# Kernel tuning notes

Measured on AMD Instinct MI355X. Metric: run time of the kernel, lower is better.

## Reference

```python
import jax, jax.numpy as jnp
import numpy as np

N, E, H = 50000, 800000, 128

def _lin_params(key, out_dim, in_dim, bias=True, gain=1.0):
    k1, k2 = jax.random.split(key)
    lim = gain * np.sqrt(6.0 / (in_dim + out_dim))
    W = jax.random.uniform(k1, (out_dim, in_dim), jnp.float32, -lim, lim)
    b = jax.random.uniform(k2, (out_dim,), jnp.float32, -lim, lim) if bias else None
    return W, b

def setup_inputs() -> dict:
    key = jax.random.key(0)
    ks = jax.random.split(key, 12)
    h = jax.random.normal(ks[0], (N, H), jnp.float32)
    x = jax.random.normal(ks[1], (N, 3), jnp.float32)
    edge_index = jax.random.randint(ks[2], (2, E), 0, N, jnp.int64)
    We1, be1 = _lin_params(ks[3], H, 2 * H + 1)
    We2, be2 = _lin_params(ks[4], H, H)
    Wn1, bn1 = _lin_params(ks[5], H, 2 * H)
    Wn2, bn2 = _lin_params(ks[6], H, H)
    Wc1, bc1 = _lin_params(ks[7], H, H)
    Wc2, _ = _lin_params(ks[8], 1, H, bias=False, gain=0.001)
    gamma = jnp.ones((H,), jnp.float32)
    beta = jnp.zeros((H,), jnp.float32)
    return {"h": h, "x": x, "edge_index": edge_index,
            "We1": We1, "be1": be1, "We2": We2, "be2": be2,
            "Wn1": Wn1, "bn1": bn1, "Wn2": Wn2, "bn2": bn2,
            "Wc1": Wc1, "bc1": bc1, "Wc2": Wc2,
            "gamma": gamma, "beta": beta}

def _layer_norm(y, gamma, beta, eps=1e-5):
    mu = jnp.mean(y, axis=-1, keepdims=True)
    var = jnp.var(y, axis=-1, keepdims=True)
    return (y - mu) * jax.lax.rsqrt(var + eps) * gamma + beta

def reference(h, x, edge_index, We1, be1, We2, be2, Wn1, bn1, Wn2, bn2,
              Wc1, bc1, Wc2, gamma, beta):
    src, dst = edge_index[0], edge_index[1]
    diff = x[src] - x[dst]                                  # (E, 3)
    dist_sq = jnp.sum(diff * diff, axis=-1, keepdims=True)  # (E, 1)
    edge_in = jnp.concatenate([h[src], h[dst], dist_sq], axis=-1)  # (E, 2H+1)
    m = jax.nn.silu(edge_in @ We1.T + be1)
    m = jax.nn.silu(m @ We2.T + be2)                        # (E, H)
    num_nodes = h.shape[0]
    agg = jax.ops.segment_sum(m, dst, num_segments=num_nodes)            # (N, H)
    count = jax.ops.segment_sum(jnp.ones((dst.shape[0], 1), h.dtype), dst,
                                num_segments=num_nodes)
    count = jnp.maximum(count, 1.0)
    agg = agg / count
    u = jax.nn.silu(jnp.concatenate([h, agg], axis=-1) @ Wn1.T + bn1)
    h_out = h + (u @ Wn2.T + bn2)
    h_out = _layer_norm(h_out, gamma, beta)
    cw = jax.nn.silu(m @ Wc1.T + bc1) @ Wc2.T               # (E, 1)
    coord_agg = jax.ops.segment_sum(diff * cw, dst, num_segments=num_nodes) / count
    x_out = x + coord_agg
    return h_out, x_out
```

## Files before the change

### kernel.cpp

```cpp
#include <hip/hip_runtime.h>
#include <stdint.h>

using bf16x8 = __attribute__((ext_vector_type(8))) short;
using f32x4  = __attribute__((ext_vector_type(4))) float;

__device__ __forceinline__ unsigned short f2bf(float f) {
  uint32_t x = __float_as_uint(f);
  x += 0x7fffu + ((x >> 16) & 1u);
  return (unsigned short)(x >> 16);
}
__device__ __forceinline__ float bf2f(unsigned short u) {
  return __uint_as_float(((uint32_t)u) << 16);
}
__device__ __forceinline__ uint32_t cvtpk2(float lo, float hi) {
  uint32_t r;
  asm("v_cvt_pk_bf16_f32 %0, %1, %2" : "=v"(r) : "v"(lo), "v"(hi));
  return r;
}
__device__ __forceinline__ float silu_f(float v) {
  float e = __expf(-v);
  return v * __builtin_amdgcn_rcpf(1.0f + e);
}
__device__ __forceinline__ void unpack2(uint32_t u, float& lo, float& hi) {
  lo = __uint_as_float(u << 16);
  hi = __uint_as_float(u & 0xffff0000u);
}

__device__ __forceinline__ int msoff(int row, int col) {
  return row * 136 + ((((col >> 3) + row * 4) & 15) << 3) + (col & 7);
}
__device__ __forceinline__ int msoff_slot(int row, int slot) {
  return row * 136 + (((slot + row * 4) & 15) << 3);
}

__global__ void prep_kernel(const float* __restrict__ We1, const float* __restrict__ We2,
                            const float* __restrict__ Wn1, const float* __restrict__ Wn2,
                            const float* __restrict__ Wc1, const int* __restrict__ ei,
                            unsigned short* __restrict__ W1p, unsigned short* __restrict__ W2b,
                            unsigned short* __restrict__ N1b, unsigned short* __restrict__ N2b,
                            unsigned short* __restrict__ W3b, float* __restrict__ w1c,
                            int* __restrict__ flag) {
  int i = blockIdx.x * 256 + threadIdx.x;
  if (i < 256 * 128) {
    int c = i >> 7, k = i & 127;
    W1p[i] = f2bf(We1[(size_t)(c & 127) * 257 + ((c >> 7) << 7) + k]);
    N1b[i] = f2bf(Wn1[i]);
  }
  if (i < 128 * 128) {
    W2b[i] = f2bf(We2[i]);
    W3b[i] = f2bf(Wc1[i]);
    N2b[i] = f2bf(Wn2[i]);
  }
  if (i < 128) w1c[i] = We1[i * 257 + 256];
  if (i == 0) {
    int allz = 1;
    for (int k = 0; k < 64; ++k) allz &= (ei[2 * k + 1] == 0);
    *flag = allz;
  }
}

__global__ void hist_kernel(const int* __restrict__ ei, const int* __restrict__ flag,
                            int* __restrict__ deg, int E) {
  int e0 = (blockIdx.x * 256 + threadIdx.x) * 2;
  if (e0 >= E) return;
  bool has1 = (e0 + 1 < E);
  int d0, d1 = 0;
  if (*flag) {
    const long long* p = (const long long*)ei + E + e0;
    d0 = (int)p[0]; if (has1) d1 = (int)p[1];
  } else {
    const int* p = ei + E + e0;
    d0 = p[0]; if (has1) d1 = p[1];
  }
  atomicAdd(&deg[d0], 1);
  if (has1) atomicAdd(&deg[d1], 1);
}

__global__ void scanA_kernel(const int* __restrict__ deg, int* __restrict__ offs,
                             int* __restrict__ bsum, int N) {
  __shared__ int sh[256];
  int t = threadIdx.x, idx = blockIdx.x * 256 + t;
  int v = (idx < N) ? deg[idx] : 0;
  sh[t] = v;
  __syncthreads();
#pragma unroll
  for (int d = 1; d < 256; d <<= 1) {
    int u = (t >= d) ? sh[t - d] : 0;
    __syncthreads();
    sh[t] += u;
    __syncthreads();
  }
  if (idx < N) offs[idx] = sh[t] - v;
  if (t == 255) bsum[blockIdx.x] = sh[255];
}

__global__ void scanB_kernel(int* __restrict__ bsum, int* __restrict__ offs,
                             int nb, int N) {
  __shared__ int sh[256];
  int t = threadIdx.x;
  int v = (t < nb) ? bsum[t] : 0;
  sh[t] = v;
  __syncthreads();
#pragma unroll
  for (int d = 1; d < 256; d <<= 1) {
    int u = (t >= d) ? sh[t - d] : 0;
    __syncthreads();
    sh[t] += u;
    __syncthreads();
  }
  bsum[t] = sh[t] - v;
  if (t == 255) offs[N] = sh[255];
}

__global__ void scanC_kernel(const int* __restrict__ bsum, int* __restrict__ offs,
                             int* __restrict__ cursor, int N) {
  int idx = blockIdx.x * 256 + threadIdx.x;
  if (idx < N) {
    int o = offs[idx] + bsum[blockIdx.x];
    offs[idx] = o;
    cursor[idx] = o;
  }
}

__global__ void scatter_kernel(const int* __restrict__ ei, const int* __restrict__ flag,
                               int* __restrict__ cursor, int2* __restrict__ sd_s, int E) {
  int e0 = (blockIdx.x * 256 + threadIdx.x) * 2;
  if (e0 >= E) return;
  int ne = min(2, E - e0);
  int ss[2], dd[2];
  if (*flag) {
    const long long* ps = (const long long*)ei + e0;
    const long long* pd = (const long long*)ei + E + e0;
    for (int j = 0; j < ne; ++j) { ss[j] = (int)ps[j]; dd[j] = (int)pd[j]; }
  } else {
    const int* ps = ei + e0;
    const int* pd = ei + E + e0;
    for (int j = 0; j < ne; ++j) { ss[j] = ps[j]; dd[j] = pd[j]; }
  }
  for (int j = 0; j < ne; ++j) {
    int pos = atomicAdd(&cursor[dd[j]], 1);
    int2 p; p.x = ss[j]; p.y = dd[j];
    sd_s[pos] = p;
  }
}

__global__ __launch_bounds__(256) void proj_kernel(
    const float* __restrict__ h, const float* __restrict__ be1,
    const unsigned short* __restrict__ W1p,
    unsigned short* __restrict__ Ps, unsigned short* __restrict__ Pd, int N) {
  const int tid = threadIdx.x;
  const int base = blockIdx.x * 64;
  const int w = tid >> 6, lane = tid & 63, lg = lane >> 4, lr = lane & 15;

  f32x4 acc[4][4];
#pragma unroll
  for (int m = 0; m < 4; ++m)
#pragma unroll
    for (int n = 0; n < 4; ++n) { f32x4 z = {0.f,0.f,0.f,0.f}; acc[m][n] = z; }

#pragma unroll
  for (int k0 = 0; k0 < 4; ++k0) {
    bf16x8 b[4];
#pragma unroll
    for (int n = 0; n < 4; ++n)
      b[n] = *(const bf16x8*)(W1p + ((w * 64 + n * 16 + lr) << 7) + k0 * 32 + lg * 8);
#pragma unroll
    for (int m = 0; m < 4; ++m) {
      int row = base + m * 16 + lr; if (row >= N) row = N - 1;
      const float* p = h + (size_t)row * 128 + k0 * 32 + lg * 8;
      float4 fa = *(const float4*)p;
      float4 fb = *(const float4*)(p + 4);
      union { uint32_t u[4]; bf16x8 v; } cv;
      cv.u[0] = cvtpk2(fa.x, fa.y); cv.u[1] = cvtpk2(fa.z, fa.w);
      cv.u[2] = cvtpk2(fb.x, fb.y); cv.u[3] = cvtpk2(fb.z, fb.w);
#pragma unroll
      for (int n = 0; n < 4; ++n)
        acc[m][n] = __builtin_amdgcn_mfma_f32_16x16x32_bf16(cv.v, b[n], acc[m][n], 0, 0, 0);
    }
  }
#pragma unroll
  for (int n = 0; n < 4; ++n) {
    int o = w * 64 + n * 16 + lr;
    unsigned short* dstp = (o < 128) ? Ps : Pd;
    int oo = o & 127;
    float add = (o < 128) ? be1[o] : 0.f;
#pragma unroll
    for (int m = 0; m < 4; ++m)
#pragma unroll
      for (int r = 0; r < 4; ++r) {
        int row = base + m * 16 + lg * 4 + r;
        if (row < N) dstp[(size_t)row * 128 + oo] = f2bf(acc[m][n][r] + add);
      }
  }
}

__global__ __launch_bounds__(256, 6) void edge_kernel(
    const unsigned short* __restrict__ Ps, const unsigned short* __restrict__ Pd,
    const float* __restrict__ x, const int2* __restrict__ sd_s,
    const int* __restrict__ offs,
    const float* __restrict__ w1c,
    const float* __restrict__ be2, const float* __restrict__ bc1,
    const float* __restrict__ Wc2,
    const unsigned short* __restrict__ W2b, const unsigned short* __restrict__ W3b,
    float* __restrict__ aggH, float* __restrict__ coordX, int E) {
  __shared__ __align__(16) unsigned short Ms[64 * 136];
  __shared__ float swred[4][64];
  __shared__ int   ssrc[64], sdst[64];
  __shared__ float sds[64];
  __shared__ float sdif[64][3];
  __shared__ unsigned char sA[64], sB[64];

  const int tid   = threadIdx.x;
  const int tbase = blockIdx.x * 64;
  const int w = tid >> 6, lane = tid & 63, lg = lane >> 4, lr = lane & 15;

  if (tid < 64) {
    int p0 = tbase + tid;
    int s = 0, d = 0;
    unsigned char fa = 0, fb = 0;
    if (p0 < E) {
      int2 p = sd_s[p0]; s = p.x; d = p.y;
      fa = (offs[d] == p0);
      fb = (offs[d + 1] == p0 + 1);
    }
    ssrc[tid] = s; sdst[tid] = d;
    sA[tid] = fa; sB[tid] = fb;
    float dx = x[s * 3 + 0] - x[d * 3 + 0];
    float dy = x[s * 3 + 1] - x[d * 3 + 1];
    float dz = x[s * 3 + 2] - x[d * 3 + 2];
    sdif[tid][0] = dx; sdif[tid][1] = dy; sdif[tid][2] = dz;
    sds[tid] = dx * dx + dy * dy + dz * dz;
  }
  __syncthreads();

  {
    const float4* w4 = (const float4*)w1c;
#pragma unroll
    for (int ch = 0; ch < 2; ++ch) {
      uint4 av[2], bv[2];
#pragma unroll
      for (int it = 0; it < 2; ++it) {
        int idx = tid + (ch * 2 + it) * 256;
        int e = idx >> 4, seg = idx & 15;
        av[it] = *(const uint4*)(Ps + (size_t)ssrc[e] * 128 + seg * 8);
        bv[it] = *(const uint4*)(Pd + (size_t)sdst[e] * 128 + seg * 8);
      }
#pragma unroll
      for (int it = 0; it < 2; ++it) {
        int idx = tid + (ch * 2 + it) * 256;
        int e = idx >> 4, seg = idx & 15;
        float dsv = sds[e];
        float4 wA = w4[seg * 2], wB = w4[seg * 2 + 1];
        float a0,a1,a2,a3,a4,a5,a6,a7, b0,b1,b2,b3,b4,b5,b6,b7;
        unpack2(((uint32_t*)&av[it])[0], a0, a1);
        unpack2(((uint32_t*)&av[it])[1], a2, a3);
        unpack2(((uint32_t*)&av[it])[2], a4, a5);
        unpack2(((uint32_t*)&av[it])[3], a6, a7);
        unpack2(((uint32_t*)&bv[it])[0], b0, b1);
        unpack2(((uint32_t*)&bv[it])[1], b2, b3);
        unpack2(((uint32_t*)&bv[it])[2], b4, b5);
        unpack2(((uint32_t*)&bv[it])[3], b6, b7);
        float v0 = silu_f(a0 + b0 + dsv * wA.x);
        float v1 = silu_f(a1 + b1 + dsv * wA.y);
        float v2 = silu_f(a2 + b2 + dsv * wA.z);
        float v3 = silu_f(a3 + b3 + dsv * wA.w);
        float v4 = silu_f(a4 + b4 + dsv * wB.x);
        float v5 = silu_f(a5 + b5 + dsv * wB.y);
        float v6 = silu_f(a6 + b6 + dsv * wB.z);
        float v7 = silu_f(a7 + b7 + dsv * wB.w);
        uint4 o;
        o.x = cvtpk2(v0, v1); o.y = cvtpk2(v2, v3);
        o.z = cvtpk2(v4, v5); o.w = cvtpk2(v6, v7);
        *(uint4*)(&Ms[msoff_slot(e, seg)]) = o;
      }
    }
  }
  __syncthreads();

  {
    f32x4 acc[4][2];
#pragma unroll
    for (int m = 0; m < 4; ++m) { f32x4 z = {0.f,0.f,0.f,0.f}; acc[m][0] = z; acc[m][1] = z; }
#pragma unroll
    for (int k0 = 0; k0 < 4; ++k0) {
      bf16x8 b0 = *(const bf16x8*)(W2b + ((w * 32 + lr)      << 7) + k0 * 32 + lg * 8);
      bf16x8 b1 = *(const bf16x8*)(W2b + ((w * 32 + 16 + lr) << 7) + k0 * 32 + lg * 8);
#pragma unroll
      for (int m = 0; m < 4; ++m) {
        int row = m * 16 + lr;
        bf16x8 a = *(const bf16x8*)(&Ms[msoff_slot(row, k0 * 4 + lg)]);
        acc[m][0] = __builtin_amdgcn_mfma_f32_16x16x32_bf16(a, b0, acc[m][0], 0, 0, 0);
        acc[m][1] = __builtin_amdgcn_mfma_f32_16x16x32_bf16(a, b1, acc[m][1], 0, 0, 0);
      }
    }
    uint32_t pk[4][2][2];
#pragma unroll
    for (int n = 0; n < 2; ++n) {
      int o = w * 32 + n * 16 + lr;
      float b2v = be2[o];
#pragma unroll
      for (int m = 0; m < 4; ++m)
#pragma unroll
        for (int r2 = 0; r2 < 4; r2 += 2)
          pk[m][n][r2 >> 1] = cvtpk2(silu_f(acc[m][n][r2] + b2v),
                                     silu_f(acc[m][n][r2 + 1] + b2v));
    }
    __syncthreads();
#pragma unroll
    for (int n = 0; n < 2; ++n) {
      int o = w * 32 + n * 16 + lr;
#pragma unroll
      for (int m = 0; m < 4; ++m)
#pragma unroll
        for (int r2 = 0; r2 < 4; r2 += 2) {
          int row = m * 16 + lg * 4 + r2;
          uint32_t u = pk[m][n][r2 >> 1];
          Ms[msoff(row, o)]     = (unsigned short)(u & 0xffffu);
          Ms[msoff(row + 1, o)] = (unsigned short)(u >> 16);
        }
    }
  }
  __syncthreads();

  {
    f32x4 acc[4][2];
#pragma unroll
    for (int m = 0; m < 4; ++m) { f32x4 z = {0.f,0.f,0.f,0.f}; acc[m][0] = z; acc[m][1] = z; }
#pragma unroll
    for (int k0 = 0; k0 < 4; ++k0) {
      bf16x8 b0 = *(const bf16x8*)(W3b + ((w * 32 + lr)      << 7) + k0 * 32 + lg * 8);
      bf16x8 b1 = *(const bf16x8*)(W3b + ((w * 32 + 16 + lr) << 7) + k0 * 32 + lg * 8);
#pragma unroll
      for (int m = 0; m < 4; ++m) {
        int row = m * 16 + lr;
        bf16x8 a = *(const bf16x8*)(&Ms[msoff_slot(row, k0 * 4 + lg)]);
        acc[m][0] = __builtin_amdgcn_mfma_f32_16x16x32_bf16(a, b0, acc[m][0], 0, 0, 0);
        acc[m][1] = __builtin_amdgcn_mfma_f32_16x16x32_bf16(a, b1, acc[m][1], 0, 0, 0);
      }
    }
    float pr[4][4];
#pragma unroll
    for (int m = 0; m < 4; ++m)
#pragma unroll
      for (int r2 = 0; r2 < 4; ++r2) pr[m][r2] = 0.f;
#pragma unroll
    for (int n = 0; n < 2; ++n) {
      int o = w * 32 + n * 16 + lr;
      float b3 = bc1[o], wc = Wc2[o];
#pragma unroll
      for (int m = 0; m < 4; ++m)
#pragma unroll
        for (int r2 = 0; r2 < 4; ++r2)
          pr[m][r2] += silu_f(acc[m][n][r2] + b3) * wc;
    }
#pragma unroll
    for (int m = 0; m < 4; ++m)
#pragma unroll
      for (int r2 = 0; r2 < 4; ++r2) {
        float v = pr[m][r2];
        v += __shfl_xor(v, 1); v += __shfl_xor(v, 2);
        v += __shfl_xor(v, 4); v += __shfl_xor(v, 8);
        pr[m][r2] = v;
      }
    if (lr == 0) {
#pragma unroll
      for (int m = 0; m < 4; ++m)
#pragma unroll
        for (int r2 = 0; r2 < 4; ++r2)
          swred[w][m * 16 + lg * 4 + r2] = pr[m][r2];
    }
  }
  __syncthreads();

  const int nv = min(64, E - tbase);
  if (tid < 128) {
    int cp = tid & 63, hf = tid >> 6;
    int c0 = cp * 2;
    int e0 = hf * 32;
    int nvh = min(32, nv - e0);
    if (nvh > 0) {
      float r0 = 0.f, r1 = 0.f;
      int prev = sdst[e0];
      int es = e0;
#pragma unroll 4
      for (int j = 0; j < nvh; ++j) {
        int e = e0 + j;
        int d = sdst[e];
        uint32_t u = *(const uint32_t*)(&Ms[msoff(e, c0)]);
        if (d != prev) {
          float* a0 = &aggH[(size_t)prev * 128 + c0];
          if (sA[es] && sB[e - 1]) { a0[0] = r0; a0[1] = r1; }
          else { atomicAdd(a0, r0); atomicAdd(a0 + 1, r1); }
          r0 = 0.f; r1 = 0.f; prev = d; es = e;
        }
        float lo, hi; unpack2(u, lo, hi);
        r0 += lo; r1 += hi;
      }
      float* a0 = &aggH[(size_t)prev * 128 + c0];
      if (sA[es] && sB[e0 + nvh - 1]) { a0[0] = r0; a0[1] = r1; }
      else { atomicAdd(a0, r0); atomicAdd(a0 + 1, r1); }
    }
  } else if (tid >= 192 && tid < 198) {
    int t6 = tid - 192;
    int c3 = t6 % 3, hf = t6 / 3;
    int e0 = hf * 32;
    int nvh = min(32, nv - e0);
    if (nvh > 0) {
      float run = 0.f;
      int prev = sdst[e0];
      int es = e0;
#pragma unroll 4
      for (int j = 0; j < nvh; ++j) {
        int e = e0 + j;
        int d = sdst[e];
        float cwv = swred[0][e] + swred[1][e] + swred[2][e] + swred[3][e];
        if (d != prev) {
          if (sA[es] && sB[e - 1]) coordX[(size_t)prev * 3 + c3] = run;
          else atomicAdd(&coordX[(size_t)prev * 3 + c3], run);
          run = 0.f; prev = d; es = e;
        }
        run += sdif[e][c3] * cwv;
      }
      if (sA[es] && sB[e0 + nvh - 1]) coordX[(size_t)prev * 3 + c3] = run;
      else atomicAdd(&coordX[(size_t)prev * 3 + c3], run);
    }
  }
}

__global__ __launch_bounds__(256) void node_kernel(
    const float* __restrict__ h, const float* __restrict__ x,
    const float* __restrict__ bn1, const float* __restrict__ bn2,
    const float* __restrict__ gamma, const float* __restrict__ beta,
    const unsigned short* __restrict__ N1b, const unsigned short* __restrict__ N2b,
    float* __restrict__ aggH, float* __restrict__ coordX,
    const int* __restrict__ deg, int N) {
  __shared__ __align__(16) unsigned short In[64][264];
  __shared__ __align__(16) unsigned short U[64][136];
  __shared__ float scnt[64];

  const int tid  = threadIdx.x;
  const int base = blockIdx.x * 64;
  const int w    = tid >> 6;
  const int lane = tid & 63;
  const int lg   = lane >> 4, lr = lane & 15;
  const int w16  = w * 16;

  if (tid < 64) {
    int n = base + tid;
    scnt[tid] = (n < N) ? fmaxf((float)deg[n], 1.0f) : 1.0f;
  }
  __syncthreads();

#pragma unroll
  for (int it = 0; it < 8; ++it) {
    int idx = tid + it * 256;
    int i = idx >> 5, seg = idx & 31;
    int n = base + i; if (n >= N) n = N - 1;
    float sc = 1.0f;
    const float* p;
    if (seg < 16) { p = h + (size_t)n * 128 + seg * 8; }
    else          { p = aggH + (size_t)n * 128 + (seg - 16) * 8; sc = 1.0f / scnt[i]; }
    float4 a = *(const float4*)p;
    float4 b = *(const float4*)(p + 4);
    uint32_t u0 = cvtpk2(a.x * sc, a.y * sc);
    uint32_t u1 = cvtpk2(a.z * sc, a.w * sc);
    uint32_t u2 = cvtpk2(b.x * sc, b.y * sc);
    uint32_t u3 = cvtpk2(b.z * sc, b.w * sc);
    uint4 v = {u0, u1, u2, u3};
    *(uint4*)&In[i][seg * 8] = v;
  }
  __syncthreads();

  {
    f32x4 acc[8];
#pragma unroll
    for (int n = 0; n < 8; ++n) { f32x4 z = {0.f,0.f,0.f,0.f}; acc[n] = z; }
#pragma unroll
    for (int k0 = 0; k0 < 8; ++k0) {
      bf16x8 a = *(const bf16x8*)(&In[w16 + lr][k0 * 32 + lg * 8]);
#pragma unroll
      for (int n = 0; n < 8; ++n) {
        bf16x8 b = *(const bf16x8*)(N1b + ((n * 16 + lr) << 8) + k0 * 32 + lg * 8);
        acc[n] = __builtin_amdgcn_mfma_f32_16x16x32_bf16(a, b, acc[n], 0, 0, 0);
      }
    }
#pragma unroll
    for (int n = 0; n < 8; ++n) {
      int o = n * 16 + lr;
      float b1 = bn1[o];
#pragma unroll
      for (int r = 0; r < 4; ++r) {
        int me = lg * 4 + r;
        U[w16 + me][o] = f2bf(silu_f(acc[n][r] + b1));
      }
    }
  }

  float* hp = (float*)&In[0][0];
  {
    f32x4 acc[8];
#pragma unroll
    for (int n = 0; n < 8; ++n) { f32x4 z = {0.f,0.f,0.f,0.f}; acc[n] = z; }
#pragma unroll
    for (int k0 = 0; k0 < 4; ++k0) {
      bf16x8 a = *(const bf16x8*)(&U[w16 + lr][k0 * 32 + lg * 8]);
#pragma unroll
      for (int n = 0; n < 8; ++n) {
        bf16x8 b = *(const bf16x8*)(N2b + ((n * 16 + lr) << 7) + k0 * 32 + lg * 8);
        acc[n] = __builtin_amdgcn_mfma_f32_16x16x32_bf16(a, b, acc[n], 0, 0, 0);
      }
    }
#pragma unroll
    for (int n = 0; n < 8; ++n) {
      int o = n * 16 + lr;
      float b2 = bn2[o];
#pragma unroll
      for (int r = 0; r < 4; ++r) {
        int me = w16 + lg * 4 + r;
        int ng = base + me; if (ng >= N) ng = N - 1;
        hp[(size_t)me * 132 + o] = acc[n][r] + b2 + h[(size_t)ng * 128 + o];
      }
    }
  }
  __syncthreads();

  {
    int r = tid >> 2, q = tid & 3;
    int ng = base + r;
    float s = 0.f, s2 = 0.f;
#pragma unroll
    for (int j = 0; j < 32; ++j) {
      float v = hp[(size_t)r * 132 + j * 4 + q];
      s += v; s2 += v * v;
    }
    s  += __shfl_xor(s, 1);  s  += __shfl_xor(s, 2);
    s2 += __shfl_xor(s2, 1); s2 += __shfl_xor(s2, 2);
    float mu  = s * (1.0f / 128.0f);
    float var = s2 * (1.0f / 128.0f) - mu * mu;
    float rs  = rsqrtf(var + 1e-5f);
    if (ng < N) {
#pragma unroll
      for (int j = 0; j < 32; ++j) {
        int o = j * 4 + q;
        float v = (hp[(size_t)r * 132 + o] - mu) * rs * gamma[o] + beta[o];
        aggH[(size_t)ng * 128 + o] = v;
      }
    }
  }

  if (tid < 192) {
    int i = tid / 3, c = tid % 3;
    int n2 = base + i;
    if (n2 < N) {
      size_t off = (size_t)n2 * 3 + c;
      coordX[off] = x[off] + coordX[off] / scnt[i];
    }
  }
}

extern "C" void kernel_launch(void* const* d_in, const int* in_sizes, int n_in,
                              void* d_out, int out_size, void* d_ws, size_t ws_size,
                              hipStream_t stream) {
  const float* h    = (const float*)d_in[0];
  const float* x    = (const float*)d_in[1];
  const int*   ei   = (const int*)d_in[2];
  const float* We1  = (const float*)d_in[3];
  const float* be1  = (const float*)d_in[4];
  const float* We2  = (const float*)d_in[5];
  const float* be2  = (const float*)d_in[6];
  const float* Wn1  = (const float*)d_in[7];
  const float* bn1  = (const float*)d_in[8];
  const float* Wn2  = (const float*)d_in[9];
  const float* bn2  = (const float*)d_in[10];
  const float* Wc1  = (const float*)d_in[11];
  const float* bc1  = (const float*)d_in[12];
  const float* Wc2  = (const float*)d_in[13];
  const float* gamma = (const float*)d_in[14];
  const float* beta  = (const float*)d_in[15];

  int N = in_sizes[0] / 128;
  int E = in_sizes[2] / 2;

  float* aggH   = (float*)d_out;
  float* coordX = (float*)d_out + (size_t)N * 128;

  char* ws = (char*)d_ws;
  size_t off = 0;
  auto alloc = [&](size_t bytes) {
    char* p = ws + off;
    off = (off + bytes + 255) & ~(size_t)255;
    return p;
  };
  unsigned short* Ps     = (unsigned short*)alloc((size_t)N * 128 * 2);
  unsigned short* Pd     = (unsigned short*)alloc((size_t)N * 128 * 2);
  unsigned short* W1p    = (unsigned short*)alloc(256 * 128 * 2);
  unsigned short* W2b    = (unsigned short*)alloc(128 * 128 * 2);
  unsigned short* N1b    = (unsigned short*)alloc(128 * 256 * 2);
  unsigned short* N2b    = (unsigned short*)alloc(128 * 128 * 2);
  unsigned short* W3b    = (unsigned short*)alloc(128 * 128 * 2);
  float*          w1c    = (float*)alloc(128 * 4);
  int*            flag   = (int*)alloc(4);
  int*            deg    = (int*)alloc((size_t)N * 4);
  int*            offs   = (int*)alloc(((size_t)N + 1) * 4);
  int*            cursor = (int*)alloc((size_t)N * 4);
  int*            bsum   = (int*)alloc(256 * 4);
  int2*           sd_s   = (int2*)alloc((size_t)E * 8);
  (void)ws_size;

  int nb = (N + 255) / 256;
  int epairs = (E + 1) / 2;

  hipMemsetAsync(d_out, 0, (size_t)out_size * 4, stream);
  hipMemsetAsync(deg, 0, (size_t)N * 4, stream);

  prep_kernel<<<128, 256, 0, stream>>>(We1, We2, Wn1, Wn2, Wc1, ei,
                                       W1p, W2b, N1b, N2b, W3b, w1c, flag);
  hist_kernel<<<(epairs + 255) / 256, 256, 0, stream>>>(ei, flag, deg, E);
  scanA_kernel<<<nb, 256, 0, stream>>>(deg, offs, bsum, N);
  scanB_kernel<<<1, 256, 0, stream>>>(bsum, offs, nb, N);
  scanC_kernel<<<nb, 256, 0, stream>>>(bsum, offs, cursor, N);
  scatter_kernel<<<(epairs + 255) / 256, 256, 0, stream>>>(ei, flag, cursor, sd_s, E);
  proj_kernel<<<(N + 63) / 64, 256, 0, stream>>>(h, be1, W1p, Ps, Pd, N);
  edge_kernel<<<(E + 63) / 64, 256, 0, stream>>>(Ps, Pd, x, sd_s, offs, w1c,
                                                 be2, bc1, Wc2, W2b, W3b,
                                                 aggH, coordX, E);
  node_kernel<<<(N + 63) / 64, 256, 0, stream>>>(h, x, bn1, bn2, gamma, beta, N1b, N2b,
                                                 aggH, coordX, deg, N);
}
```

Measured before the change: 381.7 us.

## Fold weight prep into scan, sniff index dtype per block, drop direct-store path

Removes the separate prep kernel: weight bf16 conversion moves into the first scan kernel, and the int64/int32 index detection now runs per block inside the histogram and scatter kernels through a shared-memory flag. The edge kernel stops loading segment offsets and no longer takes the plain-store path for segments fully owned by one block, so every segment uses atomics. The edge kernel's launch bound rises from 6 to 8 blocks per SM. This saves one launch and some loads and flags per edge block, at the cost of more atomic traffic and possible register pressure from the tighter occupancy bound.

```diff
diff --git a/kernel.cpp b/kernel.cpp
--- a/kernel.cpp
+++ b/kernel.cpp
@@ -33,39 +33,26 @@
   return row * 136 + (((slot + row * 4) & 15) << 3);
 }
 
-__global__ void prep_kernel(const float* __restrict__ We1, const float* __restrict__ We2,
-                            const float* __restrict__ Wn1, const float* __restrict__ Wn2,
-                            const float* __restrict__ Wc1, const int* __restrict__ ei,
-                            unsigned short* __restrict__ W1p, unsigned short* __restrict__ W2b,
-                            unsigned short* __restrict__ N1b, unsigned short* __restrict__ N2b,
-                            unsigned short* __restrict__ W3b, float* __restrict__ w1c,
-                            int* __restrict__ flag) {
-  int i = blockIdx.x * 256 + threadIdx.x;
-  if (i < 256 * 128) {
-    int c = i >> 7, k = i & 127;
-    W1p[i] = f2bf(We1[(size_t)(c & 127) * 257 + ((c >> 7) << 7) + k]);
-    N1b[i] = f2bf(Wn1[i]);
-  }
-  if (i < 128 * 128) {
-    W2b[i] = f2bf(We2[i]);
-    W3b[i] = f2bf(Wc1[i]);
-    N2b[i] = f2bf(Wn2[i]);
-  }
-  if (i < 128) w1c[i] = We1[i * 257 + 256];
-  if (i == 0) {
+__device__ __forceinline__ int sniff_int64(const int* __restrict__ ei, int E,
+                                           int* sflag_lds) {
+  if (threadIdx.x == 0) {
     int allz = 1;
-    for (int k = 0; k < 64; ++k) allz &= (ei[2 * k + 1] == 0);
-    *flag = allz;
-  }
-}
-
-__global__ void hist_kernel(const int* __restrict__ ei, const int* __restrict__ flag,
-                            int* __restrict__ deg, int E) {
+    int kk = (E < 32) ? E : 32;
+    for (int k = 0; k < kk; ++k) allz &= (ei[2 * k + 1] == 0);
+    *sflag_lds = allz;
+  }
+  __syncthreads();
+  return *sflag_lds;
+}
+
+__global__ void hist_kernel(const int* __restrict__ ei, int* __restrict__ deg, int E) {
+  __shared__ int sflag;
+  int f = sniff_int64(ei, E, &sflag);
   int e0 = (blockIdx.x * 256 + threadIdx.x) * 2;
   if (e0 >= E) return;
   bool has1 = (e0 + 1 < E);
   int d0, d1 = 0;
-  if (*flag) {
+  if (f) {
     const long long* p = (const long long*)ei + E + e0;
     d0 = (int)p[0]; if (has1) d1 = (int)p[1];
   } else {
@@ -77,7 +64,13 @@
 }
 
 __global__ void scanA_kernel(const int* __restrict__ deg, int* __restrict__ offs,
-                             int* __restrict__ bsum, int N) {
+                             int* __restrict__ bsum, int N,
+                             const float* __restrict__ We1, const float* __restrict__ We2,
+                             const float* __restrict__ Wn1, const float* __restrict__ Wn2,
+                             const float* __restrict__ Wc1,
+                             unsigned short* __restrict__ W1p, unsigned short* __restrict__ W2b,
+                             unsigned short* __restrict__ N1b, unsigned short* __restrict__ N2b,
+                             unsigned short* __restrict__ W3b, float* __restrict__ w1c) {
   __shared__ int sh[256];
   int t = threadIdx.x, idx = blockIdx.x * 256 + t;
   int v = (idx < N) ? deg[idx] : 0;
@@ -92,6 +85,21 @@
   }
   if (idx < N) offs[idx] = sh[t] - v;
   if (t == 255) bsum[blockIdx.x] = sh[255];
+
+  if (blockIdx.x < 128) {
+    int i = blockIdx.x * 256 + t;
+    {
+      int c = i >> 7, k = i & 127;
+      W1p[i] = f2bf(We1[(size_t)(c & 127) * 257 + ((c >> 7) << 7) + k]);
+      N1b[i] = f2bf(Wn1[i]);
+    }
+    if (i < 128 * 128) {
+      W2b[i] = f2bf(We2[i]);
+      W3b[i] = f2bf(Wc1[i]);
+      N2b[i] = f2bf(Wn2[i]);
+    }
+    if (i < 128) w1c[i] = We1[i * 257 + 256];
+  }
 }
 
 __global__ void scanB_kernel(int* __restrict__ bsum, int* __restrict__ offs,
@@ -122,13 +130,15 @@
   }
 }
 
-__global__ void scatter_kernel(const int* __restrict__ ei, const int* __restrict__ flag,
-                               int* __restrict__ cursor, int2* __restrict__ sd_s, int E) {
+__global__ void scatter_kernel(const int* __restrict__ ei, int* __restrict__ cursor,
+                               int2* __restrict__ sd_s, int E) {
+  __shared__ int sflag;
+  int f = sniff_int64(ei, E, &sflag);
   int e0 = (blockIdx.x * 256 + threadIdx.x) * 2;
   if (e0 >= E) return;
   int ne = min(2, E - e0);
   int ss[2], dd[2];
-  if (*flag) {
+  if (f) {
     const long long* ps = (const long long*)ei + e0;
     const long long* pd = (const long long*)ei + E + e0;
     for (int j = 0; j < ne; ++j) { ss[j] = (int)ps[j]; dd[j] = (int)pd[j]; }
@@ -194,10 +204,9 @@
   }
 }
 
-__global__ __launch_bounds__(256, 6) void edge_kernel(
+__global__ __launch_bounds__(256, 8) void edge_kernel(
     const unsigned short* __restrict__ Ps, const unsigned short* __restrict__ Pd,
     const float* __restrict__ x, const int2* __restrict__ sd_s,
-    const int* __restrict__ offs,
     const float* __restrict__ w1c,
     const float* __restrict__ be2, const float* __restrict__ bc1,
     const float* __restrict__ Wc2,
@@ -208,7 +217,6 @@
   __shared__ int   ssrc[64], sdst[64];
   __shared__ float sds[64];
   __shared__ float sdif[64][3];
-  __shared__ unsigned char sA[64], sB[64];
 
   const int tid   = threadIdx.x;
   const int tbase = blockIdx.x * 64;
@@ -217,14 +225,8 @@
   if (tid < 64) {
     int p0 = tbase + tid;
     int s = 0, d = 0;
-    unsigned char fa = 0, fb = 0;
-    if (p0 < E) {
-      int2 p = sd_s[p0]; s = p.x; d = p.y;
-      fa = (offs[d] == p0);
-      fb = (offs[d + 1] == p0 + 1);
-    }
+    if (p0 < E) { int2 p = sd_s[p0]; s = p.x; d = p.y; }
     ssrc[tid] = s; sdst[tid] = d;
-    sA[tid] = fa; sB[tid] = fb;
     float dx = x[s * 3 + 0] - x[d * 3 + 0];
     float dy = x[s * 3 + 1] - x[d * 3 + 1];
     float dz = x[s * 3 + 2] - x[d * 3 + 2];
@@ -381,24 +383,21 @@
     if (nvh > 0) {
       float r0 = 0.f, r1 = 0.f;
       int prev = sdst[e0];
-      int es = e0;
 #pragma unroll 4
       for (int j = 0; j < nvh; ++j) {
         int e = e0 + j;
         int d = sdst[e];
         uint32_t u = *(const uint32_t*)(&Ms[msoff(e, c0)]);
         if (d != prev) {
-          float* a0 = &aggH[(size_t)prev * 128 + c0];
-          if (sA[es] && sB[e - 1]) { a0[0] = r0; a0[1] = r1; }
-          else { atomicAdd(a0, r0); atomicAdd(a0 + 1, r1); }
-          r0 = 0.f; r1 = 0.f; prev = d; es = e;
+          atomicAdd(&aggH[(size_t)prev * 128 + c0],     r0);
+          atomicAdd(&aggH[(size_t)prev * 128 + c0 + 1], r1);
+          r0 = 0.f; r1 = 0.f; prev = d;
         }
         float lo, hi; unpack2(u, lo, hi);
         r0 += lo; r1 += hi;
       }
-      float* a0 = &aggH[(size_t)prev * 128 + c0];
-      if (sA[es] && sB[e0 + nvh - 1]) { a0[0] = r0; a0[1] = r1; }
-      else { atomicAdd(a0, r0); atomicAdd(a0 + 1, r1); }
+      atomicAdd(&aggH[(size_t)prev * 128 + c0],     r0);
+      atomicAdd(&aggH[(size_t)prev * 128 + c0 + 1], r1);
     }
   } else if (tid >= 192 && tid < 198) {
     int t6 = tid - 192;
@@ -408,21 +407,18 @@
     if (nvh > 0) {
       float run = 0.f;
       int prev = sdst[e0];
-      int es = e0;
 #pragma unroll 4
       for (int j = 0; j < nvh; ++j) {
         int e = e0 + j;
         int d = sdst[e];
         float cwv = swred[0][e] + swred[1][e] + swred[2][e] + swred[3][e];
         if (d != prev) {
-          if (sA[es] && sB[e - 1]) coordX[(size_t)prev * 3 + c3] = run;
-          else atomicAdd(&coordX[(size_t)prev * 3 + c3], run);
-          run = 0.f; prev = d; es = e;
+          atomicAdd(&coordX[(size_t)prev * 3 + c3], run);
+          run = 0.f; prev = d;
         }
         run += sdif[e][c3] * cwv;
       }
-      if (sA[es] && sB[e0 + nvh - 1]) coordX[(size_t)prev * 3 + c3] = run;
-      else atomicAdd(&coordX[(size_t)prev * 3 + c3], run);
+      atomicAdd(&coordX[(size_t)prev * 3 + c3], run);
     }
   }
 }
@@ -599,7 +595,6 @@
   unsigned short* N2b    = (unsigned short*)alloc(128 * 128 * 2);
   unsigned short* W3b    = (unsigned short*)alloc(128 * 128 * 2);
   float*          w1c    = (float*)alloc(128 * 4);
-  int*            flag   = (int*)alloc(4);
   int*            deg    = (int*)alloc((size_t)N * 4);
   int*            offs   = (int*)alloc(((size_t)N + 1) * 4);
   int*            cursor = (int*)alloc((size_t)N * 4);
@@ -613,15 +608,15 @@
   hipMemsetAsync(d_out, 0, (size_t)out_size * 4, stream);
   hipMemsetAsync(deg, 0, (size_t)N * 4, stream);
 
-  prep_kernel<<<128, 256, 0, stream>>>(We1, We2, Wn1, Wn2, Wc1, ei,
-                                       W1p, W2b, N1b, N2b, W3b, w1c, flag);
-  hist_kernel<<<(epairs + 255) / 256, 256, 0, stream>>>(ei, flag, deg, E);
-  scanA_kernel<<<nb, 256, 0, stream>>>(deg, offs, bsum, N);
+  hist_kernel<<<(epairs + 255) / 256, 256, 0, stream>>>(ei, deg, E);
+  scanA_kernel<<<nb, 256, 0, stream>>>(deg, offs, bsum, N,
+                                       We1, We2, Wn1, Wn2, Wc1,
+                                       W1p, W2b, N1b, N2b, W3b, w1c);
   scanB_kernel<<<1, 256, 0, stream>>>(bsum, offs, nb, N);
   scanC_kernel<<<nb, 256, 0, stream>>>(bsum, offs, cursor, N);
-  scatter_kernel<<<(epairs + 255) / 256, 256, 0, stream>>>(ei, flag, cursor, sd_s, E);
+  scatter_kernel<<<(epairs + 255) / 256, 256, 0, stream>>>(ei, cursor, sd_s, E);
   proj_kernel<<<(N + 63) / 64, 256, 0, stream>>>(h, be1, W1p, Ps, Pd, N);
-  edge_kernel<<<(E + 63) / 64, 256, 0, stream>>>(Ps, Pd, x, sd_s, offs, w1c,
+  edge_kernel<<<(E + 63) / 64, 256, 0, stream>>>(Ps, Pd, x, sd_s, w1c,
                                                  be2, bc1, Wc2, W2b, W3b,
                                                  aggH, coordX, E);
   node_kernel<<<(N + 63) / 64, 256, 0, stream>>>(h, x, bn1, bn2, gamma, beta, N1b, N2b,
```

Result: no change. 378.3 us (-0.9%).
